# Kernel optimization log

Measured on AMD Instinct MI355X. Metric: run time of the kernel, lower is better.

## Reference

```python
import jax, jax.numpy as jnp
import numpy as np

V = 30000
Y = 30000
D = 768
B = 8
N = 512
PAD_ID = 0
POS_EXPONENT = 1
NEG_INF = 1e12
LN_EPS = 1e-5


def setup_inputs() -> dict:
    key = jax.random.key(0)
    k1, k2, k3, k4, k5 = jax.random.split(key, 5)
    M_s = jax.random.randint(k1, (B, N), 0, V, dtype=jnp.int64)
    E_v = jax.random.normal(k2, (V, D), dtype=jnp.float32) * 0.02
    E_y = jax.random.normal(k3, (Y, D), dtype=jnp.float32) * 0.02
    # padding_idx=0 -> zero rows
    E_v = E_v.at[PAD_ID].set(0.0)
    E_y = E_y.at[PAD_ID].set(0.0)
    W_A = jax.random.normal(k4, (D, D), dtype=jnp.float32) * (1.0 / np.sqrt(D))
    W_O = jax.random.normal(k5, (D, D), dtype=jnp.float32) * (1.0 / np.sqrt(D))
    gamma = jnp.ones((D,), dtype=jnp.float32)
    beta = jnp.zeros((D,), dtype=jnp.float32)
    return {"M_s": M_s, "E_v": E_v, "E_y": E_y, "W_A": W_A, "W_O": W_O,
            "gamma": gamma, "beta": beta}


def positional_rep(seq_len: int, exponent: int) -> jnp.ndarray:
    idx = jnp.arange(seq_len)
    rel = (idx[None, :] - idx[:, None]).astype(jnp.float32)  # [N, N], j - i
    sign = jnp.where(rel >= 0, 1.0, -1.0)
    return sign * jnp.abs(rel) ** exponent


def layer_norm(x, gamma, beta):
    mu = jnp.mean(x, axis=-1, keepdims=True)
    var = jnp.mean((x - mu) ** 2, axis=-1, keepdims=True)
    return (x - mu) * jax.lax.rsqrt(var + LN_EPS) * gamma + beta


def reference(M_s, E_v, E_y, W_A, W_O, gamma, beta):
    # Embedding lookup (dropout is identity at eval / p=0)
    X = E_v[M_s]                                   # [B, N, D]
    Q = X                                          # self-attention mode (v_q=None)
    mask = (M_s != PAD_ID)                         # [B, N]

    # attention: logits = (Q @ W_A) @ X^T + pos_bias, mask, softmax
    logits = jnp.einsum('bnd,bmd->bnm', Q @ W_A, X)  # [B, N, N]
    logits = logits + positional_rep(X.shape[1], POS_EXPONENT)[None]
    logits = jnp.where(mask[:, None, :], logits, -NEG_INF)
    A = jax.nn.softmax(logits, axis=-1)            # [B, N, N]
    Q_c = jnp.einsum('bnm,bmd->bnd', A, X @ W_O)   # [B, N, D]

    H = layer_norm(Q_c + Q, gamma, beta)           # [B, N, D]
    y_logits = jnp.einsum('bnd,yd->bny', H, E_y)   # [B, N, Y]
    return y_logits, A
```

## Files before the change

### kernel.cpp

```cpp
#include <hip/hip_runtime.h>
#include <hip/hip_bf16.h>

using bf16 = __hip_bfloat16;
typedef __attribute__((ext_vector_type(8))) short bf16x8;
typedef __attribute__((ext_vector_type(4))) float f32x4;

#define DEV __device__ __forceinline__

#define AS1 __attribute__((address_space(1)))
#define AS3 __attribute__((address_space(3)))
#define SB  __builtin_amdgcn_sched_barrier(0)
#define BARR __builtin_amdgcn_s_barrier()
#define LG0 asm volatile("s_waitcnt lgkmcnt(0)" ::: "memory")
#define VM3 asm volatile("s_waitcnt vmcnt(3)" ::: "memory")
#define VM0 asm volatile("s_waitcnt vmcnt(0)" ::: "memory")

static constexpr int Bsz = 8, Nseq = 512, Dm = 768, Vv = 30000, Yv = 30000;
static constexpr int Ypad = 30208;
static constexpr int Tok = Bsz * Nseq;
static constexpr int NT = Dm / 32;

__global__ __launch_bounds__(512, 4)
void gemm_big(const bf16* __restrict__ Ag, const bf16* __restrict__ Bg,
              float* __restrict__ Cg)
{
    __shared__ bf16 sm[9][4096];

    int bid = blockIdx.x;
    { int cpx = gridDim.x >> 3; bid = (bid & 7) * cpx + (bid >> 3); }
    const int mT = bid & 31;
    const int nT = bid >> 5;

    const int tid  = threadIdx.x;
    const int lane = tid & 63;
    const int wid  = tid >> 6;
    const int wm   = wid >> 2;
    const int wn   = wid & 3;

    const int lr = tid >> 2;
    const int sc = ((tid & 3) ^ (lr & 3)) << 3;
    const bf16* aS  = Ag + (long)(mT * 128 + lr) * Dm + sc;
    const bf16* bS0 = Bg + (long)(nT * 256 + lr) * Dm + sc;
    const bf16* bS1 = bS0 + (long)128 * Dm;
    const int ldsW = wid << 9;

    const int fl = lane & 15;
    const int fh = lane >> 4;
    const int e0 = (fh ^ (fl & 3)) << 3;
    const int aro = (wm * 64 + fl) * 32;
    const int bro = (wn * 32 + fl) * 32;

    bf16x8 afr[4], b0r[2], b1r[2];
    f32x4 acc[4][2][2] = {};

#define STG(CI, PTR, T)                                                        \
    __builtin_amdgcn_global_load_lds((const AS1 void*)((PTR) + (T) * 32),      \
        (AS3 void*)&sm[CI][ldsW], 16, 0, 0);
#define STGG(G, T)                                                             \
    STG(3*(G) + 0, aS,  T) STG(3*(G) + 1, bS0, T) STG(3*(G) + 2, bS1, T)
#define RA(CI)                                                                 \
    _Pragma("unroll") for (int mm = 0; mm < 4; ++mm)                           \
        afr[mm] = *(const bf16x8*)&sm[CI][aro + mm * 512 + e0];
#define RB(BR, CI)                                                             \
    _Pragma("unroll") for (int nn = 0; nn < 2; ++nn)                           \
        BR[nn] = *(const bf16x8*)&sm[CI][bro + nn * 512 + e0];
#define RG(G)  RA(3*(G)) RB(b0r, 3*(G)+1) RB(b1r, 3*(G)+2)
#define MF16                                                                   \
    __builtin_amdgcn_s_setprio(1);                                             \
    _Pragma("unroll") for (int mm = 0; mm < 4; ++mm)                           \
    _Pragma("unroll") for (int nn = 0; nn < 2; ++nn)                           \
        acc[mm][0][nn] = __builtin_amdgcn_mfma_f32_16x16x32_bf16(              \
            afr[mm], b0r[nn], acc[mm][0][nn], 0, 0, 0);                        \
    _Pragma("unroll") for (int mm = 0; mm < 4; ++mm)                           \
    _Pragma("unroll") for (int nn = 0; nn < 2; ++nn)                           \
        acc[mm][1][nn] = __builtin_amdgcn_mfma_f32_16x16x32_bf16(              \
            afr[mm], b1r[nn], acc[mm][1][nn], 0, 0, 0);                        \
    __builtin_amdgcn_s_setprio(0);

    STGG(0, 0) STGG(1, 1)
    VM3; SB; BARR; SB;

#pragma unroll 1
    for (int t = 0; t < NT - 3; t += 3) {
        RG(0)
        STGG(2, t + 2)
        VM3; SB; BARR; LG0; SB;
        MF16
        SB; BARR; SB;
        RG(1)
        STGG(0, t + 3)
        VM3; SB; BARR; LG0; SB;
        MF16
        SB; BARR; SB;
        RG(2)
        STGG(1, t + 4)
        VM3; SB; BARR; LG0; SB;
        MF16
        SB; BARR; SB;
    }

    {
        RG(0)
        STGG(2, NT - 1)
        VM3; SB; BARR; LG0; SB;
        MF16
        SB; BARR; SB;
        RG(1)
        VM0; SB; BARR; LG0; SB;
        MF16
        SB; BARR; SB;
        RG(2)
        SB; LG0; SB;
        MF16
    }

    const int rB = mT * 128 + wm * 64 + fh * 4;
    const int cB = nT * 256 + wn * 32 + fl;
#pragma unroll
    for (int mm = 0; mm < 4; ++mm)
#pragma unroll
    for (int nq = 0; nq < 2; ++nq)
#pragma unroll
    for (int nn = 0; nn < 2; ++nn) {
        const int c = cB + nq * 128 + nn * 16;
        if (c >= Yv) continue;
        const int r = rB + mm * 16;
#pragma unroll
        for (int j = 0; j < 4; ++j)
            __builtin_nontemporal_store(acc[mm][nq][nn][j],
                                        Cg + (long)(r + j) * Yv + c);
    }
#undef STG
#undef STGG
#undef RA
#undef RB
#undef RG
#undef MF16
}

template<bool STORE_BF16>
DEV void gemm_core(bf16* __restrict__ smem,
                   const bf16* __restrict__ A, const bf16* __restrict__ Bm,
                   void* __restrict__ Cg, int bid, int M, int K,
                   int lda, int ldb, int ldc)
{
    bf16* As = smem;
    bf16* Bs = smem + 128 * 32;

    const int nTilesM = M >> 7;
    const int mTile = bid % nTilesM;
    const int nTile = bid / nTilesM;

    const int tid  = threadIdx.x;
    const int wave = tid >> 6;
    const int lane = tid & 63;

    const int sRow = (wave << 4) + (lane >> 2);
    const int sCol = (lane & 3) << 3;

    const long aBase = (long)(mTile * 128) * lda;
    const long bBase = (long)(nTile * 128) * ldb;

    const int fl = lane & 15;
    const int fh = lane >> 4;
    const int wRow = (wave >> 1) << 6;
    const int wCol = (wave & 1) << 6;

    f32x4 acc[4][4] = {};

    for (int k0 = 0; k0 < K; k0 += 32) {
#pragma unroll
        for (int t = 0; t < 2; ++t) {
            const bf16* gA = A  + aBase + (long)(t * 64 + sRow) * lda + (k0 + sCol);
            const bf16* gB = Bm + bBase + (long)(t * 64 + sRow) * ldb + (k0 + sCol);
            bf16* lA = &As[(t * 64 + (wave << 4)) * 32];
            bf16* lB = &Bs[(t * 64 + (wave << 4)) * 32];
            __builtin_amdgcn_global_load_lds(
                (const AS1 void*)gA, (AS3 void*)lA, 16, 0, 0);
            __builtin_amdgcn_global_load_lds(
                (const AS1 void*)gB, (AS3 void*)lB, 16, 0, 0);
        }
        __syncthreads();

        bf16x8 af[4], bfg[4];
#pragma unroll
        for (int m = 0; m < 4; ++m)
            af[m] = *(const bf16x8*)&As[(wRow + m * 16 + fl) * 32 + fh * 8];
#pragma unroll
        for (int n = 0; n < 4; ++n)
            bfg[n] = *(const bf16x8*)&Bs[(wCol + n * 16 + fl) * 32 + fh * 8];
#pragma unroll
        for (int m = 0; m < 4; ++m)
#pragma unroll
            for (int n = 0; n < 4; ++n)
                acc[m][n] = __builtin_amdgcn_mfma_f32_16x16x32_bf16(
                    af[m], bfg[n], acc[m][n], 0, 0, 0);
        __syncthreads();
    }

    const int rBase = mTile * 128 + wRow + fh * 4;
    const int cBase = nTile * 128 + wCol + fl;
#pragma unroll
    for (int m = 0; m < 4; ++m) {
#pragma unroll
        for (int n = 0; n < 4; ++n) {
            int gc = cBase + n * 16;
            int gr = rBase + m * 16;
            if (STORE_BF16) {
                bf16* C = (bf16*)Cg;
#pragma unroll
                for (int j = 0; j < 4; ++j)
                    C[(long)(gr + j) * ldc + gc] = __float2bfloat16(acc[m][n][j]);
            } else {
                float* C = (float*)Cg;
#pragma unroll
                for (int j = 0; j < 4; ++j)
                    C[(long)(gr + j) * ldc + gc] = acc[m][n][j];
            }
        }
    }
}

template<bool STORE_BF16>
__global__ __launch_bounds__(256)
void gemm_bt(const bf16* __restrict__ Ag, const bf16* __restrict__ Bg,
             void* __restrict__ Cg, int M, int K,
             int lda, int ldb, int ldc, long sA, long sB, long sC)
{
    __shared__ bf16 smem[128 * 32 * 2];
    const int bz = blockIdx.z;
    char* C = (char*)Cg + (long)bz * sC * (STORE_BF16 ? 2 : 4);
    gemm_core<STORE_BF16>(smem, Ag + (long)bz * sA, Bg + (long)bz * sB,
                          (void*)C, blockIdx.x, M, K, lda, ldb, ldc);
}

__global__ __launch_bounds__(256)
void gemm_dual(const bf16* __restrict__ Xb, const bf16* __restrict__ Wcat,
               bf16* __restrict__ QWb, bf16* __restrict__ XWoT)
{
    __shared__ bf16 smem[128 * 32 * 2];
    const int bid = blockIdx.x;
    if (bid < 192)
        gemm_core<true>(smem, Xb, Wcat, (void*)QWb, bid, Tok, Dm, Dm, Dm, Dm);
    else
        gemm_core<true>(smem, Wcat + (size_t)Dm * Dm, Xb, (void*)XWoT,
                        bid - 192, Dm, Dm, Dm, Dm, Tok);
}

__global__ __launch_bounds__(256)
void gemm_bt64(const bf16* __restrict__ Ag, const bf16* __restrict__ Bg,
               bf16* __restrict__ Cg, int M, int K, int lda, int ldc,
               long sA, long sB, long sC)
{
    __shared__ bf16 As[64 * 32];
    __shared__ bf16 Bs[128 * 32];

    const int bz = blockIdx.z;
    const bf16* A  = Ag + (long)bz * sA;
    const bf16* Bm = Bg + (long)bz * sB;
    bf16* C = Cg + (long)bz * sC;

    const int bid = blockIdx.x;
    const int nTilesM = M >> 6;
    const int mTile = bid % nTilesM;
    const int nTile = bid / nTilesM;

    const int tid  = threadIdx.x;
    const int wave = tid >> 6;
    const int lane = tid & 63;

    const int sRow = tid >> 2;
    const int sCol = (tid & 3) << 3;

    const long aBase = (long)(mTile * 64) * lda;
    const long bBase = (long)(nTile * 128) * K;

    const int fl = lane & 15;
    const int fh = lane >> 4;

    f32x4 acc[4][2] = {};

    for (int k0 = 0; k0 < K; k0 += 32) {
        __builtin_amdgcn_global_load_lds(
            (const AS1 void*)(A + aBase + (long)sRow * lda + (k0 + sCol)),
            (AS3 void*)&As[wave * 512], 16, 0, 0);
#pragma unroll
        for (int t = 0; t < 2; ++t)
            __builtin_amdgcn_global_load_lds(
                (const AS1 void*)(Bm + bBase + (long)(t * 64 + sRow) * K + (k0 + sCol)),
                (AS3 void*)&Bs[t * 2048 + wave * 512], 16, 0, 0);
        __syncthreads();

        bf16x8 af[4], bfg[2];
#pragma unroll
        for (int m = 0; m < 4; ++m)
            af[m] = *(const bf16x8*)&As[(m * 16 + fl) * 32 + fh * 8];
#pragma unroll
        for (int n = 0; n < 2; ++n)
            bfg[n] = *(const bf16x8*)&Bs[(wave * 32 + n * 16 + fl) * 32 + fh * 8];
#pragma unroll
        for (int m = 0; m < 4; ++m)
#pragma unroll
            for (int n = 0; n < 2; ++n)
                acc[m][n] = __builtin_amdgcn_mfma_f32_16x16x32_bf16(
                    af[m], bfg[n], acc[m][n], 0, 0, 0);
        __syncthreads();
    }

    const int rBase = mTile * 64 + fh * 4;
    const int cBase = nTile * 128 + wave * 32 + fl;
#pragma unroll
    for (int m = 0; m < 4; ++m)
#pragma unroll
    for (int n = 0; n < 2; ++n) {
        const int gc = cBase + n * 16;
        const int gr = rBase + m * 16;
#pragma unroll
        for (int j = 0; j < 4; ++j)
            C[(long)(gr + j) * ldc + gc] = __float2bfloat16(acc[m][n][j]);
    }
}

static constexpr int PREP_CVT = 11328, PREP_WT = 1152, PREP_GATHER = 4096;

__global__ __launch_bounds__(256)
void k_prep(const float* __restrict__ Ey, bf16* __restrict__ Eyb,
            const float* __restrict__ WA, const float* __restrict__ WO,
            bf16* __restrict__ Wcat,
            const int* __restrict__ Ms, const float* __restrict__ Ev,
            bf16* __restrict__ Xb)
{
    __shared__ float t[32][33];
    const int b = blockIdx.x;
    const int tid = threadIdx.x;

    if (b < PREP_CVT) {
        const long idx = ((long)b * 256 + tid) * 8;
        const int row = (int)(idx / Dm);
        union { bf16 h[8]; uint4 u; } pk;
        if (row < Yv) {
            const f32x4* s = (const f32x4*)(Ey + idx);
            f32x4 a = __builtin_nontemporal_load(s);
            f32x4 c = __builtin_nontemporal_load(s + 1);
#pragma unroll
            for (int i = 0; i < 4; ++i) {
                pk.h[i]     = __float2bfloat16(a[i]);
                pk.h[4 + i] = __float2bfloat16(c[i]);
            }
        } else {
#pragma unroll
            for (int i = 0; i < 8; ++i) pk.h[i] = __float2bfloat16(0.f);
        }
        *(uint4*)(Eyb + idx) = pk.u;
    } else if (b < PREP_CVT + PREP_WT) {
        const int rem = b - PREP_CVT;
        const int z = rem / 576, r2 = rem % 576;
        const int bx = (r2 % 24) * 32, by = (r2 / 24) * 32;
        const float* W = z ? WO : WA;
        bf16* WT = Wcat + (size_t)z * Dm * Dm;
        const int tx = tid & 31, ty = tid >> 5;
#pragma unroll
        for (int i = 0; i < 32; i += 8)
            t[ty + i][tx] = W[(long)(bx + ty + i) * Dm + (by + tx)];
        __syncthreads();
#pragma unroll
        for (int i = 0; i < 32; i += 8)
            WT[(long)(by + ty + i) * Dm + (bx + tx)] = __float2bfloat16(t[tx][ty + i]);
    } else {
        const int token = b - (PREP_CVT + PREP_WT);
        if (tid < 192) {
            const int id = Ms[token];
            const int d = tid * 4;
            float4 v = *(const float4*)(Ev + (long)id * Dm + d);
            union { bf16 h[4]; uint2 u; } pk;
            pk.h[0] = __float2bfloat16(v.x); pk.h[1] = __float2bfloat16(v.y);
            pk.h[2] = __float2bfloat16(v.z); pk.h[3] = __float2bfloat16(v.w);
            *(uint2*)(Xb + (long)token * Dm + d) = pk.u;
        }
    }
}

DEV float waveMax(float v) {
#pragma unroll
    for (int o = 32; o > 0; o >>= 1) v = fmaxf(v, __shfl_xor(v, o, 64));
    return v;
}
DEV float waveSum(float v) {
#pragma unroll
    for (int o = 32; o > 0; o >>= 1) v += __shfl_xor(v, o, 64);
    return v;
}

__global__ __launch_bounds__(256) void k_softmax(const bf16* __restrict__ L,
                                                 const int* __restrict__ Ms,
                                                 float* __restrict__ Aout,
                                                 bf16* __restrict__ Ab)
{
    __shared__ float red[8];
    int row = blockIdx.x;
    int b = row >> 9, i = row & 511;
    const bf16* l = L + (long)row * Nseq;
    const int* ms = Ms + (b << 9);
    int t = threadIdx.x;
    int wid = t >> 6, lane = t & 63;
    int j0 = t, j1 = t + 256;

    float a0 = __bfloat162float(l[j0]) + (float)(j0 - i);
    float a1 = __bfloat162float(l[j1]) + (float)(j1 - i);
    if (ms[j0] == 0) a0 = -1e12f;
    if (ms[j1] == 0) a1 = -1e12f;

    float m = waveMax(fmaxf(a0, a1));
    if (lane == 0) red[wid] = m;
    __syncthreads();
    m = fmaxf(fmaxf(red[0], red[1]), fmaxf(red[2], red[3]));

    float e0 = expf(a0 - m), e1 = expf(a1 - m);
    float s = waveSum(e0 + e1);
    if (lane == 0) red[4 + wid] = s;
    __syncthreads();
    s = red[4] + red[5] + red[6] + red[7];
    float inv = 1.0f / s;

    float r0 = e0 * inv, r1 = e1 * inv;
    __builtin_nontemporal_store(r0, &Aout[(long)row * Nseq + j0]);
    __builtin_nontemporal_store(r1, &Aout[(long)row * Nseq + j1]);
    Ab[(long)row * Nseq + j0] = __float2bfloat16(r0);
    Ab[(long)row * Nseq + j1] = __float2bfloat16(r1);
}

__global__ __launch_bounds__(256) void k_ln(const bf16* __restrict__ Qc,
                                            const bf16* __restrict__ Xb,
                                            const float* __restrict__ gamma,
                                            const float* __restrict__ beta,
                                            bf16* __restrict__ Hb)
{
    __shared__ float red[8];
    int row = blockIdx.x;
    const bf16* q = Qc + (long)row * Dm;
    const bf16* e = Xb + (long)row * Dm;
    int t = threadIdx.x;
    int wid = t >> 6, lane = t & 63;

    float x[3];
#pragma unroll
    for (int c = 0; c < 3; ++c)
        x[c] = __bfloat162float(q[t + c * 256]) + __bfloat162float(e[t + c * 256]);

    float s = waveSum(x[0] + x[1] + x[2]);
    if (lane == 0) red[wid] = s;
    __syncthreads();
    float mu = (red[0] + red[1] + red[2] + red[3]) * (1.0f / 768.0f);

    float vs = 0.f;
#pragma unroll
    for (int c = 0; c < 3; ++c) { float d = x[c] - mu; vs += d * d; }
    vs = waveSum(vs);
    if (lane == 0) red[4 + wid] = vs;
    __syncthreads();
    float var = (red[4] + red[5] + red[6] + red[7]) * (1.0f / 768.0f);
    float rstd = rsqrtf(var + 1e-5f);

#pragma unroll
    for (int c = 0; c < 3; ++c) {
        int d = t + c * 256;
        Hb[(long)row * Dm + d] =
            __float2bfloat16((x[c] - mu) * rstd * gamma[d] + beta[d]);
    }
}

extern "C" void kernel_launch(void* const* d_in, const int* in_sizes, int n_in,
                              void* d_out, int out_size, void* d_ws, size_t ws_size,
                              hipStream_t stream)
{
    const int*   Ms    = (const int*)d_in[0];
    const float* Ev    = (const float*)d_in[1];
    const float* Ey    = (const float*)d_in[2];
    const float* WA    = (const float*)d_in[3];
    const float* WO    = (const float*)d_in[4];
    const float* gamma = (const float*)d_in[5];
    const float* beta  = (const float*)d_in[6];

    float* y_out = (float*)d_out;
    float* A_out = y_out + (size_t)Tok * Yv;

    char* ws = (char*)d_ws;
    size_t off = 0;
    auto alloc = [&](size_t n) { char* p = ws + off; off += (n + 255) & ~(size_t)255; return p; };
    bf16*  Xb    = (bf16*) alloc((size_t)Tok * Dm * 2);
    bf16*  WcatT = (bf16*) alloc((size_t)2 * Dm * Dm * 2);
    bf16*  QWb   = (bf16*) alloc((size_t)Tok * Dm * 2);
    bf16*  XWoT  = (bf16*) alloc((size_t)Dm * Tok * 2);
    bf16*  Lb    = (bf16*) alloc((size_t)Tok * Nseq * 2);
    bf16*  Ab    = (bf16*) alloc((size_t)Tok * Nseq * 2);
    bf16*  Qcb   = (bf16*) alloc((size_t)Tok * Dm * 2);
    bf16*  Hb    = (bf16*) alloc((size_t)Tok * Dm * 2);
    bf16*  Eyb   = (bf16*) alloc((size_t)Ypad * Dm * 2);

    k_prep<<<dim3(PREP_CVT + PREP_WT + PREP_GATHER), dim3(256), 0, stream>>>(
        Ey, Eyb, WA, WO, WcatT, Ms, Ev, Xb);
    gemm_dual<<<dim3(384), dim3(256), 0, stream>>>(Xb, WcatT, QWb, XWoT);
    gemm_bt64<<<dim3(32, 1, 8), dim3(256), 0, stream>>>(
        QWb, Xb, Lb, Nseq, Dm, Dm, Nseq,
        (long)Nseq * Dm, (long)Nseq * Dm, (long)Nseq * Nseq);
    k_softmax<<<dim3(Tok), dim3(256), 0, stream>>>(Lb, Ms, A_out, Ab);
    gemm_bt<true><<<dim3(24, 1, 8), dim3(256), 0, stream>>>(
        Ab, XWoT, (void*)Qcb, Nseq, Nseq, Nseq, Tok, Dm,
        (long)Nseq * Nseq, (long)Nseq, (long)Nseq * Dm);
    k_ln<<<dim3(Tok), dim3(256), 0, stream>>>(Qcb, Xb, gamma, beta, Hb);
    gemm_big<<<dim3(32 * (Ypad / 256)), dim3(512), 0, stream>>>(Hb, Eyb, y_out);
}
```

Baseline: 339.5 us.

## Load A operand directly from global into registers, bypassing LDS staging

In the large output GEMM, the A-tile fragments now go straight from global memory into VGPRs instead of being staged through LDS. Only the two B tiles stay on the triple-buffered LDS ring, which shrinks shared memory from 9 to 6 buffers and may allow more resident blocks. The cost is that the four waves sharing the same A rows each fetch them redundantly through cache. Because the direct loads are issued just before the vmcnt wait that precedes the MFMAs, their latency may no longer be hidden.

```diff
diff --git a/kernel.cpp b/kernel.cpp
--- a/kernel.cpp
+++ b/kernel.cpp
@@ -12,7 +12,7 @@
 #define SB  __builtin_amdgcn_sched_barrier(0)
 #define BARR __builtin_amdgcn_s_barrier()
 #define LG0 asm volatile("s_waitcnt lgkmcnt(0)" ::: "memory")
-#define VM3 asm volatile("s_waitcnt vmcnt(3)" ::: "memory")
+#define VM2 asm volatile("s_waitcnt vmcnt(2)" ::: "memory")
 #define VM0 asm volatile("s_waitcnt vmcnt(0)" ::: "memory")
 
 static constexpr int Bsz = 8, Nseq = 512, Dm = 768, Vv = 30000, Yv = 30000;
@@ -24,7 +24,7 @@
 void gemm_big(const bf16* __restrict__ Ag, const bf16* __restrict__ Bg,
               float* __restrict__ Cg)
 {
-    __shared__ bf16 sm[9][4096];
+    __shared__ bf16 sm[6][4096];
 
     int bid = blockIdx.x;
     { int cpx = gridDim.x >> 3; bid = (bid & 7) * cpx + (bid >> 3); }
@@ -39,7 +39,6 @@
 
     const int lr = tid >> 2;
     const int sc = ((tid & 3) ^ (lr & 3)) << 3;
-    const bf16* aS  = Ag + (long)(mT * 128 + lr) * Dm + sc;
     const bf16* bS0 = Bg + (long)(nT * 256 + lr) * Dm + sc;
     const bf16* bS1 = bS0 + (long)128 * Dm;
     const int ldsW = wid << 9;
@@ -47,8 +46,9 @@
     const int fl = lane & 15;
     const int fh = lane >> 4;
     const int e0 = (fh ^ (fl & 3)) << 3;
-    const int aro = (wm * 64 + fl) * 32;
     const int bro = (wn * 32 + fl) * 32;
+
+    const bf16* aF = Ag + (long)(mT * 128 + wm * 64 + fl) * Dm + fh * 8;
 
     bf16x8 afr[4], b0r[2], b1r[2];
     f32x4 acc[4][2][2] = {};
@@ -56,15 +56,14 @@
 #define STG(CI, PTR, T)                                                        \
     __builtin_amdgcn_global_load_lds((const AS1 void*)((PTR) + (T) * 32),      \
         (AS3 void*)&sm[CI][ldsW], 16, 0, 0);
-#define STGG(G, T)                                                             \
-    STG(3*(G) + 0, aS,  T) STG(3*(G) + 1, bS0, T) STG(3*(G) + 2, bS1, T)
-#define RA(CI)                                                                 \
+#define STGG(G, T)  STG(2*(G), bS0, T) STG(2*(G) + 1, bS1, T)
+#define AF(T)                                                                  \
     _Pragma("unroll") for (int mm = 0; mm < 4; ++mm)                           \
-        afr[mm] = *(const bf16x8*)&sm[CI][aro + mm * 512 + e0];
+        afr[mm] = *(const bf16x8*)(aF + (long)(mm * 16) * Dm + (T) * 32);
 #define RB(BR, CI)                                                             \
     _Pragma("unroll") for (int nn = 0; nn < 2; ++nn)                           \
         BR[nn] = *(const bf16x8*)&sm[CI][bro + nn * 512 + e0];
-#define RG(G)  RA(3*(G)) RB(b0r, 3*(G)+1) RB(b1r, 3*(G)+2)
+#define RGB(G)  RB(b0r, 2*(G)) RB(b1r, 2*(G)+1)
 #define MF16                                                                   \
     __builtin_amdgcn_s_setprio(1);                                             \
     _Pragma("unroll") for (int mm = 0; mm < 4; ++mm)                           \
@@ -78,39 +77,45 @@
     __builtin_amdgcn_s_setprio(0);
 
     STGG(0, 0) STGG(1, 1)
-    VM3; SB; BARR; SB;
+    VM2; SB; BARR; SB;
 
 #pragma unroll 1
     for (int t = 0; t < NT - 3; t += 3) {
-        RG(0)
+        AF(t)
+        RGB(0)
         STGG(2, t + 2)
-        VM3; SB; BARR; LG0; SB;
+        VM2; SB; BARR; LG0; SB;
         MF16
         SB; BARR; SB;
-        RG(1)
+        AF(t + 1)
+        RGB(1)
         STGG(0, t + 3)
-        VM3; SB; BARR; LG0; SB;
+        VM2; SB; BARR; LG0; SB;
         MF16
         SB; BARR; SB;
-        RG(2)
+        AF(t + 2)
+        RGB(2)
         STGG(1, t + 4)
-        VM3; SB; BARR; LG0; SB;
+        VM2; SB; BARR; LG0; SB;
         MF16
         SB; BARR; SB;
     }
 
     {
-        RG(0)
+        AF(NT - 3)
+        RGB(0)
         STGG(2, NT - 1)
-        VM3; SB; BARR; LG0; SB;
+        VM2; SB; BARR; LG0; SB;
         MF16
         SB; BARR; SB;
-        RG(1)
+        AF(NT - 2)
+        RGB(1)
         VM0; SB; BARR; LG0; SB;
         MF16
         SB; BARR; SB;
-        RG(2)
-        SB; LG0; SB;
+        AF(NT - 1)
+        RGB(2)
+        VM0; SB; LG0; SB;
         MF16
     }
 
@@ -132,9 +137,9 @@
     }
 #undef STG
 #undef STGG
-#undef RA
+#undef AF
 #undef RB
-#undef RG
+#undef RGB
 #undef MF16
 }
 
```

Measured after the change: 549.0 us. 61.7% more time.
